# Kernel optimization log

Hardware: AMD Instinct MI355X
Metric: run time of the kernel (lower is better)

The kernel has to match this reference:

```python
import jax, jax.numpy as jnp
import numpy as np


def reference(x, coef_ref, coef_qry):
    # x: [B, Hr, Wr, Hq, Wq] similarity tensor
    B, Hr, Wr, Hq, Wq = x.shape
    xr = x.reshape(B, Hr * Wr, Hq * Wq)  # [B, R, Q]
    # softmax over ref axis (axis=1) of coef_ref * (x - max over axis 1)
    xm_ref = xr - jnp.max(xr, axis=1, keepdims=True)
    conf_ref = jax.nn.softmax(coef_ref[0] * xm_ref, axis=1)
    # softmax over qry axis (axis=2) of coef_qry * (x - max over axis 2)
    xm_qry = xr - jnp.max(xr, axis=2, keepdims=True)
    conf_qry = jax.nn.softmax(coef_qry[0] * xm_qry, axis=2)
    confidence = jnp.sqrt(conf_ref * conf_qry)  # [B, R, Q]
    # top_k(k=1) over last axis + gather_nd of that value == max over axis 2
    values = jnp.max(confidence, axis=2)  # [B, R]
    return values.reshape(B, Hr, Wr, 1)


def setup_inputs() -> dict:
    key = jax.random.key(0)
    k1, = jax.random.split(key, 1)
    B, Hr, Wr, Hq, Wq = 16, 64, 64, 32, 32
    alpha = 10.0
    x = jax.random.normal(k1, (B, Hr, Wr, Hq, Wq), dtype=jnp.float32)
    coef_ref = jnp.full((1,), alpha, dtype=jnp.float32)
    coef_qry = jnp.full((1,), alpha, dtype=jnp.float32)
    return {"x": x, "coef_ref": coef_ref, "coef_qry": coef_qry}
```

## Files before the change

### kernel.cpp

```cpp
#include <hip/hip_runtime.h>
#include <math.h>
#include <stdint.h>


constexpr int B = 16;
constexpr int R = 4096;
constexpr int Q = 1024;
constexpr int CAP = 32;
#define DTH 0.80f

__device__ __forceinline__ float wmax64(float v) {
#pragma unroll
    for (int o = 32; o; o >>= 1) v = fmaxf(v, __shfl_xor(v, o, 64));
    return v;
}
__device__ __forceinline__ float max4(float4 v) {
    return fmaxf(fmaxf(v.x, v.y), fmaxf(v.z, v.w));
}

__global__ __launch_bounds__(256) void qatm_sample(const float* __restrict__ x,
                                                   float* __restrict__ rmSamp) {
    const int b = blockIdx.x >> 3, k = blockIdx.x & 7;
    const int t = threadIdx.x;
    const float4* xr = reinterpret_cast<const float4*>(x) +
                       ((size_t)b * R + (size_t)k * 512) * (Q / 4);
    float m = wmax64(max4(xr[t]));
    __shared__ float sh[4];
    if ((t & 63) == 0) sh[t >> 6] = m;
    __syncthreads();
    if (t == 0)
        rmSamp[blockIdx.x] = fmaxf(fmaxf(sh[0], sh[1]), fmaxf(sh[2], sh[3]));
}

__global__ __launch_bounds__(256) void qatm_pass1(
    const float* __restrict__ x,
    float* __restrict__ psum,
    float* __restrict__ rsArr,
    uint32_t* __restrict__ cntArr,
    float4* __restrict__ cand4,
    uint32_t* __restrict__ candg,
    const float* __restrict__ rmSamp,
    float* __restrict__ thOut,
    const float* __restrict__ coef_ref,
    const float* __restrict__ coef_qry)
{
    const int blk = blockIdx.x;
    const int b = blk >> 6, chunk = blk & 63;
    const int t = threadIdx.x;
    const float ar = coef_ref[0], aq = coef_qry[0];
    const bool same = (ar == aq);
    float thsum = 0.f;
#pragma unroll
    for (int i = 0; i < 8; ++i) thsum += rmSamp[b * 8 + i];
    const float th = thsum * 0.125f - DTH;
    if (chunk == 0 && t == 0) thOut[b] = th;

    const size_t row0 = (size_t)b * R + (size_t)chunk * 64;
    const float4* xb = reinterpret_cast<const float4*>(x) + row0 * (Q / 4) + t;

    __shared__ float ssum[16][256];
    __shared__ int cnt_sh[16];
    if (t < 16) cnt_sh[t] = 0;
    __syncthreads();

    float4 cs = {0.f, 0.f, 0.f, 0.f};

    for (int win = 0; win < 4; ++win) {
#pragma unroll 4
        for (int rr = 0; rr < 16; ++rr) {
            const int r = win * 16 + rr;
            float4 v = xb[(size_t)r * 256];
            float4 e;
            e.x = __expf(ar * v.x); e.y = __expf(ar * v.y);
            e.z = __expf(ar * v.z); e.w = __expf(ar * v.w);
            cs.x += e.x; cs.y += e.y; cs.z += e.z; cs.w += e.w;
            float rp;
            if (same) rp = (e.x + e.y) + (e.z + e.w);
            else rp = (__expf(aq * v.x) + __expf(aq * v.y)) +
                      (__expf(aq * v.z) + __expf(aq * v.w));
            ssum[rr][t] = rp;
            if (max4(v) >= th) {
                int idx = atomicAdd(&cnt_sh[rr], 1);
                if (idx < CAP) {
                    const size_t grow = row0 + r;
                    cand4[grow * CAP + idx] = v;
                    candg[grow * CAP + idx] = (uint32_t)t;
                }
            }
        }
        __syncthreads();
        const int j = t >> 4, s = t & 15;
        float p = 0.f;
#pragma unroll
        for (int i = 0; i < 16; ++i) p += ssum[j][i * 16 + s];
        p += __shfl_xor(p, 1, 64);
        p += __shfl_xor(p, 2, 64);
        p += __shfl_xor(p, 4, 64);
        p += __shfl_xor(p, 8, 64);
        if (s == 0) {
            const size_t grow = row0 + win * 16 + j;
            rsArr[grow] = p;
            cntArr[grow] = (uint32_t)cnt_sh[j];
            cnt_sh[j] = 0;
        }
        __syncthreads();
    }
    reinterpret_cast<float4*>(psum)[(size_t)blk * 256 + t] = cs;
}

__global__ __launch_bounds__(256) void qatm_combine(
    const float* __restrict__ psum, float* __restrict__ cvec,
    float* __restrict__ cminArr)
{
    const int b = blockIdx.x, t = threadIdx.x;
    float4 s = {0.f, 0.f, 0.f, 0.f};
    const float4* p = reinterpret_cast<const float4*>(psum) + (size_t)b * 64 * 256 + t;
#pragma unroll 16
    for (int i = 0; i < 64; ++i) {
        float4 v = p[(size_t)i * 256];
        s.x += v.x; s.y += v.y; s.z += v.z; s.w += v.w;
    }
    float4 c;
    c.x = __logf(s.x); c.y = __logf(s.y); c.z = __logf(s.z); c.w = __logf(s.w);
    reinterpret_cast<float4*>(cvec)[b * 256 + t] = c;
    float m = fminf(fminf(c.x, c.y), fminf(c.z, c.w));
    m = -wmax64(-m);
    __shared__ float sh[4];
    if ((t & 63) == 0) sh[t >> 6] = m;
    __syncthreads();
    if (t == 0) cminArr[b] = fminf(fminf(sh[0], sh[1]), fminf(sh[2], sh[3]));
}

__global__ __launch_bounds__(256) void qatm_select(
    const float* __restrict__ x, const float* __restrict__ cvec,
    const float* __restrict__ cminArr, const float* __restrict__ thArr,
    const float* __restrict__ rsArr, const uint32_t* __restrict__ cntArr,
    const float4* __restrict__ cand4, const uint32_t* __restrict__ candg,
    const float* __restrict__ coef_ref, const float* __restrict__ coef_qry,
    float* __restrict__ out)
{
    const int w = threadIdx.x >> 6, l = threadIdx.x & 63;
    const size_t row = (size_t)blockIdx.x * 4 + w;
    const int b = (int)(row >> 12);
    const float ar = coef_ref[0], aq = coef_qry[0], s2 = ar + aq;
    const uint32_t cnt = cntArr[row];
    const float rs = rsArr[row];

    float best = -INFINITY;
    bool fb = (cnt > CAP) || (cnt == 0) || !(s2 > 0.f);
    if (!fb) {
        if (l < (int)cnt) {
            float4 v = cand4[row * CAP + l];
            uint32_t g = candg[row * CAP + l];
            float4 c = reinterpret_cast<const float4*>(cvec)[((size_t)b << 8) + g];
            best = fmaxf(fmaxf(s2 * v.x - c.x, s2 * v.y - c.y),
                         fmaxf(s2 * v.z - c.z, s2 * v.w - c.w));
        }
        best = wmax64(best);
        if (!(best >= s2 * thArr[b] - cminArr[b])) fb = true;
    }
    if (fb) {
        const float4* xr = reinterpret_cast<const float4*>(x) + row * (Q / 4);
        const float4* cq = reinterpret_cast<const float4*>(cvec) + ((size_t)b << 8);
        best = -INFINITY;
#pragma unroll
        for (int it = 0; it < 4; ++it) {
            float4 v = xr[it * 64 + l], c = cq[it * 64 + l];
            best = fmaxf(best, fmaxf(fmaxf(s2 * v.x - c.x, s2 * v.y - c.y),
                                     fmaxf(s2 * v.z - c.z, s2 * v.w - c.w)));
        }
        best = wmax64(best);
    }
    if (l == 0) out[row] = __expf(0.5f * (best - __logf(rs)));
}

extern "C" void kernel_launch(void* const* d_in, const int* in_sizes, int n_in,
                              void* d_out, int out_size, void* d_ws, size_t ws_size,
                              hipStream_t stream) {
    const float* x = (const float*)d_in[0];
    const float* coef_ref = (const float*)d_in[1];
    const float* coef_qry = (const float*)d_in[2];
    float* out = (float*)d_out;

    char* ws = (char*)d_ws;
    size_t off = 0;
    float4*   cand4 = (float4*)(ws + off);   off += (size_t)B * R * CAP * 16;
    float*    psum  = (float*)(ws + off);    off += (size_t)B * 64 * 1024 * 4;
    uint32_t* candg = (uint32_t*)(ws + off); off += (size_t)B * R * CAP * 4;
    float*    cvec  = (float*)(ws + off);    off += (size_t)B * Q * 4;
    float*    rsA   = (float*)(ws + off);    off += (size_t)B * R * 4;
    uint32_t* cntA  = (uint32_t*)(ws + off); off += (size_t)B * R * 4;
    float*    rmSamp= (float*)(ws + off);    off += 512;
    float*    thA   = (float*)(ws + off);    off += 64;
    float*    cmin  = (float*)(ws + off);    off += 64;

    qatm_sample<<<B * 8, 256, 0, stream>>>(x, rmSamp);
    qatm_pass1<<<B * 64, 256, 0, stream>>>(x, psum, rsA, cntA, cand4, candg,
                                           rmSamp, thA, coef_ref, coef_qry);
    qatm_combine<<<B, 256, 0, stream>>>(psum, cvec, cmin);
    qatm_select<<<(B * R) / 4, 256, 0, stream>>>(x, cvec, cmin, thA, rsA, cntA,
                                                 cand4, candg, coef_ref, coef_qry, out);
}
```

Before: 94.19 us.

## Batch nontemporal loads in pass1, widen combine grid, pack row sum and count

The pass1 inner loop now issues eight nontemporal vector loads up front before doing any exp work on them, which raises memory-level parallelism and avoids polluting the cache with streamed data. The combine kernel goes from 16 to 64 blocks, each owning one column quarter, and merges the per-batch minimum through an order-preserving encoded atomicMin whose slot is initialized in the sample kernel. Row sum and candidate count are packed into one float2 so select does a single load per row. The cost is more registers for the batched loads and an extra atomic step, and correctness now depends on the sample kernel initializing the min slot before combine runs.

```diff
diff --git a/kernel.cpp b/kernel.cpp
--- a/kernel.cpp
+++ b/kernel.cpp
@@ -9,6 +9,8 @@
 constexpr int CAP = 32;
 #define DTH 0.80f
 
+typedef float float4n __attribute__((ext_vector_type(4)));
+
 __device__ __forceinline__ float wmax64(float v) {
 #pragma unroll
     for (int o = 32; o; o >>= 1) v = fmaxf(v, __shfl_xor(v, o, 64));
@@ -17,11 +19,22 @@
 __device__ __forceinline__ float max4(float4 v) {
     return fmaxf(fmaxf(v.x, v.y), fmaxf(v.z, v.w));
 }
+__device__ __forceinline__ uint32_t encf(float f) {
+    uint32_t u = __float_as_uint(f);
+    return (u & 0x80000000u) ? ~u : (u | 0x80000000u);
+}
+__device__ __forceinline__ float decf(uint32_t e) {
+    uint32_t u = (e & 0x80000000u) ? (e & 0x7FFFFFFFu) : ~e;
+    return __uint_as_float(u);
+}
 
 __global__ __launch_bounds__(256) void qatm_sample(const float* __restrict__ x,
-                                                   float* __restrict__ rmSamp) {
-    const int b = blockIdx.x >> 3, k = blockIdx.x & 7;
+                                                   float* __restrict__ rmSamp,
+                                                   uint32_t* __restrict__ cminEnc) {
+    const int blk = blockIdx.x;
+    const int b = blk >> 3, k = blk & 7;
     const int t = threadIdx.x;
+    if ((blk & 7) == 0 && t == 0) cminEnc[b] = 0xFFFFFFFFu;
     const float4* xr = reinterpret_cast<const float4*>(x) +
                        ((size_t)b * R + (size_t)k * 512) * (Q / 4);
     float m = wmax64(max4(xr[t]));
@@ -29,14 +42,13 @@
     if ((t & 63) == 0) sh[t >> 6] = m;
     __syncthreads();
     if (t == 0)
-        rmSamp[blockIdx.x] = fmaxf(fmaxf(sh[0], sh[1]), fmaxf(sh[2], sh[3]));
+        rmSamp[blk] = fmaxf(fmaxf(sh[0], sh[1]), fmaxf(sh[2], sh[3]));
 }
 
 __global__ __launch_bounds__(256) void qatm_pass1(
     const float* __restrict__ x,
     float* __restrict__ psum,
-    float* __restrict__ rsArr,
-    uint32_t* __restrict__ cntArr,
+    float2* __restrict__ rscnt,
     float4* __restrict__ cand4,
     uint32_t* __restrict__ candg,
     const float* __restrict__ rmSamp,
@@ -56,7 +68,7 @@
     if (chunk == 0 && t == 0) thOut[b] = th;
 
     const size_t row0 = (size_t)b * R + (size_t)chunk * 64;
-    const float4* xb = reinterpret_cast<const float4*>(x) + row0 * (Q / 4) + t;
+    const float4n* xb = reinterpret_cast<const float4n*>(x) + row0 * (Q / 4) + t;
 
     __shared__ float ssum[16][256];
     __shared__ int cnt_sh[16];
@@ -66,25 +78,33 @@
     float4 cs = {0.f, 0.f, 0.f, 0.f};
 
     for (int win = 0; win < 4; ++win) {
-#pragma unroll 4
-        for (int rr = 0; rr < 16; ++rr) {
-            const int r = win * 16 + rr;
-            float4 v = xb[(size_t)r * 256];
-            float4 e;
-            e.x = __expf(ar * v.x); e.y = __expf(ar * v.y);
-            e.z = __expf(ar * v.z); e.w = __expf(ar * v.w);
-            cs.x += e.x; cs.y += e.y; cs.z += e.z; cs.w += e.w;
-            float rp;
-            if (same) rp = (e.x + e.y) + (e.z + e.w);
-            else rp = (__expf(aq * v.x) + __expf(aq * v.y)) +
-                      (__expf(aq * v.z) + __expf(aq * v.w));
-            ssum[rr][t] = rp;
-            if (max4(v) >= th) {
-                int idx = atomicAdd(&cnt_sh[rr], 1);
-                if (idx < CAP) {
-                    const size_t grow = row0 + r;
-                    cand4[grow * CAP + idx] = v;
-                    candg[grow * CAP + idx] = (uint32_t)t;
+        const float4n* xw = xb + (size_t)win * 16 * 256;
+#pragma unroll
+        for (int rr8 = 0; rr8 < 16; rr8 += 8) {
+            float4n vn[8];
+#pragma unroll
+            for (int k = 0; k < 8; ++k)
+                vn[k] = __builtin_nontemporal_load(&xw[(size_t)(rr8 + k) * 256]);
+#pragma unroll
+            for (int k = 0; k < 8; ++k) {
+                const int rr = rr8 + k;
+                float4 v = make_float4(vn[k].x, vn[k].y, vn[k].z, vn[k].w);
+                float4 e;
+                e.x = __expf(ar * v.x); e.y = __expf(ar * v.y);
+                e.z = __expf(ar * v.z); e.w = __expf(ar * v.w);
+                cs.x += e.x; cs.y += e.y; cs.z += e.z; cs.w += e.w;
+                float rp;
+                if (same) rp = (e.x + e.y) + (e.z + e.w);
+                else rp = (__expf(aq * v.x) + __expf(aq * v.y)) +
+                          (__expf(aq * v.z) + __expf(aq * v.w));
+                ssum[rr][t] = rp;
+                if (max4(v) >= th) {
+                    int idx = atomicAdd(&cnt_sh[rr], 1);
+                    if (idx < CAP) {
+                        const size_t grow = row0 + win * 16 + rr;
+                        cand4[grow * CAP + idx] = v;
+                        candg[grow * CAP + idx] = (uint32_t)t;
+                    }
                 }
             }
         }
@@ -99,8 +119,7 @@
         p += __shfl_xor(p, 8, 64);
         if (s == 0) {
             const size_t grow = row0 + win * 16 + j;
-            rsArr[grow] = p;
-            cntArr[grow] = (uint32_t)cnt_sh[j];
+            rscnt[grow] = make_float2(p, __uint_as_float((uint32_t)cnt_sh[j]));
             cnt_sh[j] = 0;
         }
         __syncthreads();
@@ -110,31 +129,31 @@
 
 __global__ __launch_bounds__(256) void qatm_combine(
     const float* __restrict__ psum, float* __restrict__ cvec,
-    float* __restrict__ cminArr)
+    uint32_t* __restrict__ cminEnc)
 {
-    const int b = blockIdx.x, t = threadIdx.x;
-    float4 s = {0.f, 0.f, 0.f, 0.f};
-    const float4* p = reinterpret_cast<const float4*>(psum) + (size_t)b * 64 * 256 + t;
+    const int b = blockIdx.x >> 2, part = blockIdx.x & 3;
+    const int t = threadIdx.x;
+    const int col = part * 256 + t;
+    float s = 0.f;
+    const float* p = psum + (size_t)b * 64 * 1024 + col;
 #pragma unroll 16
-    for (int i = 0; i < 64; ++i) {
-        float4 v = p[(size_t)i * 256];
-        s.x += v.x; s.y += v.y; s.z += v.z; s.w += v.w;
-    }
-    float4 c;
-    c.x = __logf(s.x); c.y = __logf(s.y); c.z = __logf(s.z); c.w = __logf(s.w);
-    reinterpret_cast<float4*>(cvec)[b * 256 + t] = c;
-    float m = fminf(fminf(c.x, c.y), fminf(c.z, c.w));
-    m = -wmax64(-m);
+    for (int i = 0; i < 64; ++i) s += p[(size_t)i * 1024];
+    const float c = __logf(s);
+    cvec[b * 1024 + col] = c;
+    float m = -wmax64(-c);
     __shared__ float sh[4];
     if ((t & 63) == 0) sh[t >> 6] = m;
     __syncthreads();
-    if (t == 0) cminArr[b] = fminf(fminf(sh[0], sh[1]), fminf(sh[2], sh[3]));
+    if (t == 0) {
+        float mm = fminf(fminf(sh[0], sh[1]), fminf(sh[2], sh[3]));
+        atomicMin(&cminEnc[b], encf(mm));
+    }
 }
 
 __global__ __launch_bounds__(256) void qatm_select(
     const float* __restrict__ x, const float* __restrict__ cvec,
-    const float* __restrict__ cminArr, const float* __restrict__ thArr,
-    const float* __restrict__ rsArr, const uint32_t* __restrict__ cntArr,
+    const uint32_t* __restrict__ cminEnc, const float* __restrict__ thArr,
+    const float2* __restrict__ rscnt,
     const float4* __restrict__ cand4, const uint32_t* __restrict__ candg,
     const float* __restrict__ coef_ref, const float* __restrict__ coef_qry,
     float* __restrict__ out)
@@ -143,8 +162,9 @@
     const size_t row = (size_t)blockIdx.x * 4 + w;
     const int b = (int)(row >> 12);
     const float ar = coef_ref[0], aq = coef_qry[0], s2 = ar + aq;
-    const uint32_t cnt = cntArr[row];
-    const float rs = rsArr[row];
+    const float2 rc = rscnt[row];
+    const float rs = rc.x;
+    const uint32_t cnt = __float_as_uint(rc.y);
 
     float best = -INFINITY;
     bool fb = (cnt > CAP) || (cnt == 0) || !(s2 > 0.f);
@@ -157,7 +177,7 @@
                          fmaxf(s2 * v.z - c.z, s2 * v.w - c.w));
         }
         best = wmax64(best);
-        if (!(best >= s2 * thArr[b] - cminArr[b])) fb = true;
+        if (!(best >= s2 * thArr[b] - decf(cminEnc[b]))) fb = true;
     }
     if (fb) {
         const float4* xr = reinterpret_cast<const float4*>(x) + row * (Q / 4);
@@ -188,16 +208,15 @@
     float*    psum  = (float*)(ws + off);    off += (size_t)B * 64 * 1024 * 4;
     uint32_t* candg = (uint32_t*)(ws + off); off += (size_t)B * R * CAP * 4;
     float*    cvec  = (float*)(ws + off);    off += (size_t)B * Q * 4;
-    float*    rsA   = (float*)(ws + off);    off += (size_t)B * R * 4;
-    uint32_t* cntA  = (uint32_t*)(ws + off); off += (size_t)B * R * 4;
+    float2*   rscnt = (float2*)(ws + off);   off += (size_t)B * R * 8;
     float*    rmSamp= (float*)(ws + off);    off += 512;
     float*    thA   = (float*)(ws + off);    off += 64;
-    float*    cmin  = (float*)(ws + off);    off += 64;
-
-    qatm_sample<<<B * 8, 256, 0, stream>>>(x, rmSamp);
-    qatm_pass1<<<B * 64, 256, 0, stream>>>(x, psum, rsA, cntA, cand4, candg,
+    uint32_t* cminE = (uint32_t*)(ws + off); off += 64;
+
+    qatm_sample<<<B * 8, 256, 0, stream>>>(x, rmSamp, cminE);
+    qatm_pass1<<<B * 64, 256, 0, stream>>>(x, psum, rscnt, cand4, candg,
                                            rmSamp, thA, coef_ref, coef_qry);
-    qatm_combine<<<B, 256, 0, stream>>>(psum, cvec, cmin);
-    qatm_select<<<(B * R) / 4, 256, 0, stream>>>(x, cvec, cmin, thA, rsA, cntA,
+    qatm_combine<<<64, 256, 0, stream>>>(psum, cvec, cminE);
+    qatm_select<<<(B * R) / 4, 256, 0, stream>>>(x, cvec, cminE, thA, rscnt,
                                                  cand4, candg, coef_ref, coef_qry, out);
 }
```

Result: faster. 88.95 us (-5.6%).
